# Kernel tuning notes

Hardware: AMD Instinct MI355X
Metric: run time of the kernel (lower is better)

## Reference

```python
import jax, jax.numpy as jnp
import numpy as np

B, N, NT, C, CO = 8, 12288, 3072, 256, 512
H0, W0 = 128, 96

def _grid_idx(loc, h, w):
    # loc in [-1,1] -> nearest grid cell index (matches token2map's round/clamp)
    loc = jnp.clip(jax.lax.stop_gradient(loc), -1.0, 1.0)
    xi = jnp.clip(jnp.round(0.5 * (loc[..., 0] + 1.0) * w - 0.5).astype(jnp.int32), 0, w - 1)
    yi = jnp.clip(jnp.round(0.5 * (loc[..., 1] + 1.0) * h - 0.5).astype(jnp.int32), 0, h - 1)
    return xi + yi * w

def _bn(x, gamma, beta):
    # BatchNorm (training-mode batch stats) over (B, N) per channel; x: (B, N, C)
    mean = x.mean(axis=(0, 1))
    var = ((x - mean) ** 2).mean(axis=(0, 1))
    return (x - mean) * jax.lax.rsqrt(var + 1e-5) * gamma + beta

def _token2map(x, loc, idx_agg, h, w):
    b, n, c = x.shape
    n0 = idx_agg.shape[1]
    seg = (_grid_idx(loc, h, w) + jnp.arange(b)[:, None] * (h * w)).reshape(-1)
    x_pt = jnp.take_along_axis(x, idx_agg[..., None], axis=1).reshape(b * n0, c)
    summed = jax.ops.segment_sum(x_pt, seg, num_segments=b * h * w)
    count = jax.ops.segment_sum(jnp.ones((b * n0,), x.dtype), seg, num_segments=b * h * w)
    x_map = summed / (count + 1e-6)[:, None]
    return x_map.reshape(b, h, w, c).transpose(0, 3, 1, 2)  # (B, C, H, W)

def _map2token(fmap, nt, loc, idx_agg_t, agg_weight_t):
    b, c, h, w = fmap.shape
    n0 = idx_agg_t.shape[1]
    idx_hw = _grid_idx(loc, h, w)
    fflat = fmap.reshape(b, c, h * w).transpose(0, 2, 1)  # (B, HW, C)
    feat = jnp.take_along_axis(fflat, idx_hw[..., None], axis=1)  # (B, N0, C)
    wgt = agg_weight_t.reshape(b, n0)
    seg = (idx_agg_t + jnp.arange(b)[:, None] * nt).reshape(-1)
    num = jax.ops.segment_sum((feat * wgt[..., None]).reshape(b * n0, c), seg, num_segments=b * nt)
    den = jax.ops.segment_sum(wgt.reshape(-1), seg, num_segments=b * nt) + 1e-6
    return (num / den[:, None]).reshape(b, nt, c)

def _token_downup(x_s, idx_agg_s, nt, idx_agg_t, agg_weight_t):
    b, s, c = x_s.shape
    n0 = idx_agg_s.shape[1]
    x_pt = jnp.take_along_axis(x_s, idx_agg_s[..., None], axis=1)  # (B, N0, C)
    wgt = agg_weight_t.reshape(b, n0)
    seg = (idx_agg_t + jnp.arange(b)[:, None] * nt).reshape(-1)
    num = jax.ops.segment_sum((x_pt * wgt[..., None]).reshape(b * n0, c), seg, num_segments=b * nt)
    den = jax.ops.segment_sum(wgt.reshape(-1), seg, num_segments=b * nt) + 1e-6
    return (num / den[:, None]).reshape(b, nt, c)

def setup_inputs():
    key = jax.random.key(0)
    ks = jax.random.split(key, 10)
    return {
        "x": jax.random.normal(ks[0], (B, N, C), jnp.float32),
        "loc_orig": jax.random.uniform(ks[1], (B, N, 2), jnp.float32, -1.0, 1.0),
        "idx_agg": jax.random.randint(ks[2], (B, N), 0, N),
        "agg_weight": jax.random.uniform(ks[3], (B, N, 1), jnp.float32),
        "x_t": jax.random.normal(ks[4], (B, NT, C), jnp.float32),
        "idx_agg_t": jax.random.randint(ks[5], (B, N), 0, NT),
        "agg_weight_t": jax.random.uniform(ks[6], (B, N, 1), jnp.float32),
        "H": H0, "W": W0,
        "dw_conv_w": jax.random.normal(ks[7], (C, 1, 3, 3), jnp.float32) * 0.1,
        "dw_skip_w": jax.random.normal(ks[8], (C, 1, 1, 1), jnp.float32) * 0.1,
        "norm1_gamma": jnp.ones((C,), jnp.float32),
        "norm1_beta": jnp.zeros((C,), jnp.float32),
        "conv_w": jax.random.normal(ks[9], (CO, C), jnp.float32) * (1.0 / np.sqrt(C)),
        "norm2_gamma": jnp.ones((CO,), jnp.float32),
        "norm2_beta": jnp.zeros((CO,), jnp.float32),
    }

def reference(x, loc_orig, idx_agg, agg_weight, x_t, idx_agg_t, agg_weight_t, H, W,
              dw_conv_w, dw_skip_w, norm1_gamma, norm1_beta, conv_w, norm2_gamma, norm2_beta):
    nt = x_t.shape[1]
    # token2map -> depthwise 3x3 stride-2 conv -> map2token (onto downsampled grid)
    x_map = _token2map(x, loc_orig, idx_agg, H, W)
    x_map = jax.lax.conv_general_dilated(
        x_map, dw_conv_w, window_strides=(2, 2), padding=((1, 1), (1, 1)),
        feature_group_count=x_map.shape[1],
        dimension_numbers=("NCHW", "OIHW", "NCHW"))
    x_map = _map2token(x_map, nt, loc_orig, idx_agg_t, agg_weight_t)
    # skip path: token_downup + 1x1 depthwise (per-channel scale)
    xd = _token_downup(x, idx_agg, nt, idx_agg_t, agg_weight_t)
    xd = xd * dw_skip_w.reshape(1, 1, -1)
    xd = xd + x_map
    xd = _bn(xd, norm1_gamma, norm1_beta)
    xd = jnp.einsum("bnc,oc->bno", xd, conv_w)  # 1x1 conv C -> CO
    xd = _bn(xd, norm2_gamma, norm2_beta)
    return jax.nn.relu(xd)
```

## Files before the change

### kernel.cpp

```cpp
#include <hip/hip_runtime.h>
#include <hip/hip_bf16.h>

using bf16 = __hip_bfloat16;
typedef __attribute__((ext_vector_type(8))) short bf16x8;
typedef __attribute__((ext_vector_type(4))) float f32x4;

#define BB   8
#define NN   12288
#define NTOK (BB*NN)
#define NTK  3072
#define CC   256
#define CCO  512
#define HH   128
#define WWI  96
#define HWIN (HH*WWI)
#define H2   64
#define W2   48
#define HW2  (H2*W2)
#define RR   (BB*NTK)

#define O_CONV  0LL
#define O_XD    6291456LL
#define O_AUX   9437184LL
#define O_WT    12582912LL
#define O_ST1   12713984LL
#define O_ST2   12714496LL
#define O_AB1   12715520LL
#define O_B2    12716032LL
#define O_AB2   12716544LL
#define O_FLAG  12717568LL
#define O_META  12717572LL
#define O_OFF   12914180LL
#define O_LIST  13037060LL

__device__ __forceinline__ float cvt(float v){ return v; }
__device__ __forceinline__ float cvt(bf16 v){ return __bfloat162float(v); }
template<typename T>
__device__ __forceinline__ float ld(const void* p, long long i){
    return cvt(((const T*)p)[i]);
}
__device__ __forceinline__ float bfu(unsigned short u){
    return __uint_as_float((unsigned)u << 16);
}
__device__ __forceinline__ unsigned short ubf(float f){
    bf16 h = __float2bfloat16(f);
    return *(unsigned short*)&h;
}
template<typename T>
__device__ __forceinline__ f32x4 ld4(const void* p, long long i);
template<>
__device__ __forceinline__ f32x4 ld4<bf16>(const void* p, long long i){
    const ushort4 u = *(const ushort4*)((const unsigned short*)p + i);
    return (f32x4){bfu(u.x), bfu(u.y), bfu(u.z), bfu(u.w)};
}
template<>
__device__ __forceinline__ f32x4 ld4<float>(const void* p, long long i){
    const float4 v = *(const float4*)((const float*)p + i);
    return (f32x4){v.x, v.y, v.z, v.w};
}

__global__ void k_flag(const float* __restrict__ locf, float* __restrict__ flag){
    if (threadIdx.x == 0){
        int bad = 0;
        for (int i = 0; i < 64; ++i){
            const float v = locf[i];
            if (!(v >= -1.0f && v <= 1.0f)) bad = 1;
        }
        flag[0] = bad ? 1.0f : 0.0f;
    }
}

__device__ __forceinline__ int2 gidx2(float lx, float ly, int h, int w){
    lx = fminf(fmaxf(lx, -1.f), 1.f);
    ly = fminf(fmaxf(ly, -1.f), 1.f);
    int xi = (int)rintf(0.5f*(lx+1.f)*(float)w - 0.5f);
    int yi = (int)rintf(0.5f*(ly+1.f)*(float)h - 0.5f);
    xi = min(max(xi,0), w-1); yi = min(max(yi,0), h-1);
    return make_int2(xi, yi);
}

template<typename T>
__device__ void meta_body(const void* loc, const int* __restrict__ iat, const void* wt,
                          int2* __restrict__ meta, int* __restrict__ off){
    const int tok = blockIdx.x*256 + threadIdx.x;
    const int b = tok / NN;
    const float lx = ld<T>(loc, 2LL*tok);
    const float ly = ld<T>(loc, 2LL*tok + 1);
    const int2 g1 = gidx2(lx, ly, HH, WWI);
    const int2 g2 = gidx2(lx, ly, H2, W2);
    const float wv = ld<T>(wt, tok);
    int2 m; m.x = g2.x + g2.y*W2; m.y = __float_as_int(wv);
    meta[tok] = m;
    atomicAdd(&off[b*HWIN + g1.x + g1.y*WWI], 1);
    atomicAdd(&off[NTOK + b*NTK + iat[tok]], 1);
}
__global__ __launch_bounds__(256) void k_meta(
        const void* loc, const int* __restrict__ iat, const void* wt,
        const float* __restrict__ flag, int2* __restrict__ meta,
        int* __restrict__ off){
    if (flag[0] != 0.0f) meta_body<bf16>(loc, iat, wt, meta, off);
    else                 meta_body<float>(loc, iat, wt, meta, off);
}

#define SCN  (NTOK + RR)
#define SCB  120
__global__ __launch_bounds__(1024) void k_scan1(int* __restrict__ off, int* __restrict__ aux){
    __shared__ int sm[1024];
    const int tid = threadIdx.x;
    const int gid = blockIdx.x*1024 + tid;
    const int v = off[gid];
    sm[tid] = v;
    __syncthreads();
    for (int d = 1; d < 1024; d <<= 1){
        const int t = (tid >= d) ? sm[tid-d] : 0;
        __syncthreads();
        sm[tid] += t;
        __syncthreads();
    }
    off[gid] = sm[tid] - v;
    if (tid == 1023) aux[blockIdx.x] = sm[1023];
}
__global__ __launch_bounds__(128) void k_scan2(int* __restrict__ aux){
    __shared__ int sm[128];
    const int tid = threadIdx.x;
    const int v = (tid < SCB) ? aux[tid] : 0;
    sm[tid] = v;
    __syncthreads();
    for (int d = 1; d < 128; d <<= 1){
        const int t = (tid >= d) ? sm[tid-d] : 0;
        __syncthreads();
        sm[tid] += t;
        __syncthreads();
    }
    if (tid < SCB) aux[tid] = sm[tid] - v;
}
__global__ __launch_bounds__(1024) void k_scan3(int* __restrict__ off, const int* __restrict__ aux){
    off[blockIdx.x*1024 + threadIdx.x] += aux[blockIdx.x];
}

template<typename T>
__device__ void fill_body(const void* loc, const int* __restrict__ ia,
                          const int* __restrict__ iat,
                          int* __restrict__ off, int* __restrict__ list){
    const int tok = blockIdx.x*256 + threadIdx.x;
    const int b = tok / NN;
    const float lx = ld<T>(loc, 2LL*tok);
    const float ly = ld<T>(loc, 2LL*tok + 1);
    const int2 g1 = gidx2(lx, ly, HH, WWI);
    const int pa = atomicAdd(&off[b*HWIN + g1.x + g1.y*WWI], 1);
    list[pa] = b*NN + ia[tok];
    const int pb = atomicAdd(&off[NTOK + b*NTK + iat[tok]], 1);
    list[pb] = tok;
}
__global__ __launch_bounds__(256) void k_fill(
        const void* loc, const int* __restrict__ ia, const int* __restrict__ iat,
        const float* __restrict__ flag,
        int* __restrict__ off, int* __restrict__ list){
    if (flag[0] != 0.0f) fill_body<bf16>(loc, ia, iat, off, list);
    else                 fill_body<float>(loc, ia, iat, off, list);
}

template<typename T>
__device__ void conv_body(const void* x, const void* dww,
                          const int* __restrict__ off, const int* __restrict__ list,
                          bf16* __restrict__ conv){
    __shared__ f32x4 red[3][64];
    const int tid = threadIdx.x;
    const int kh = tid >> 6;
    const int lane = tid & 63;
    const int ch0 = lane*4;
    const int cell = blockIdx.x;
    const int b = cell / HW2;
    const int p = cell % HW2;
    const int oh = p / W2, ow = p % W2;
    const int ih = 2*oh - 1 + kh;
    f32x4 part = (f32x4){0.f,0.f,0.f,0.f};
    if (ih >= 0){
        const int gbase = b*HWIN + ih*WWI + 2*ow - 1;
        const int e0 = (gbase >= 0) ? off[gbase] : 0;
        const int e1 = off[gbase+1];
        const int e2 = off[gbase+2];
        const int ms = (ow > 0) ? off[gbase-1] : e0;
        f32x4 w0, w1, w2;
        #pragma unroll
        for (int c = 0; c < 4; ++c){
            w0[c] = ld<T>(dww, (long long)(ch0+c)*9 + kh*3 + 0);
            w1[c] = ld<T>(dww, (long long)(ch0+c)*9 + kh*3 + 1);
            w2[c] = ld<T>(dww, (long long)(ch0+c)*9 + kh*3 + 2);
        }
        f32x4 b0 = (f32x4){0.f,0.f,0.f,0.f};
        f32x4 b1 = (f32x4){0.f,0.f,0.f,0.f};
        f32x4 b2 = (f32x4){0.f,0.f,0.f,0.f};
        int idx = ms;
        while (idx < e2){
            const int cnt = min(e2 - idx, 64);
            const int tokv = (lane < cnt) ? list[idx + lane] : 0;
            int j = 0;
            for (; j + 4 <= cnt; j += 4){
                int oxs[4];
                #pragma unroll
                for (int u = 0; u < 4; ++u)
                    oxs[u] = __shfl(tokv, j+u)*CC + ch0;
                f32x4 xv[4];
                #pragma unroll
                for (int u = 0; u < 4; ++u) xv[u] = ld4<T>(x, (long long)oxs[u]);
                #pragma unroll
                for (int u = 0; u < 4; ++u){
                    const int gi = idx + j + u;
                    if (gi < e0)      b0 += xv[u];
                    else if (gi < e1) b1 += xv[u];
                    else              b2 += xv[u];
                }
            }
            for (; j < cnt; ++j){
                const f32x4 xv = ld4<T>(x, (long long)(__shfl(tokv, j)*CC + ch0));
                const int gi = idx + j;
                if (gi < e0)      b0 += xv;
                else if (gi < e1) b1 += xv;
                else              b2 += xv;
            }
            idx += cnt;
        }
        const float r0 = 1.0f/((float)(e0 - ms) + 1e-6f);
        const float r1 = 1.0f/((float)(e1 - e0) + 1e-6f);
        const float r2 = 1.0f/((float)(e2 - e1) + 1e-6f);
        #pragma unroll
        for (int c = 0; c < 4; ++c)
            part[c] = w0[c]*b0[c]*r0 + w1[c]*b1[c]*r1 + w2[c]*b2[c]*r2;
    }
    red[kh][lane] = part;
    __syncthreads();
    if (kh == 0){
        const f32x4 t0 = red[0][lane];
        const f32x4 t1 = red[1][lane];
        const f32x4 t2 = red[2][lane];
        ushort4 o;
        o.x = ubf(t0[0]+t1[0]+t2[0]);
        o.y = ubf(t0[1]+t1[1]+t2[1]);
        o.z = ubf(t0[2]+t1[2]+t2[2]);
        o.w = ubf(t0[3]+t1[3]+t2[3]);
        *(ushort4*)((unsigned short*)conv + (long long)cell*CC + ch0) = o;
    }
}
__global__ __launch_bounds__(192) void k_conv(
        const void* x, const void* dww, const float* __restrict__ flag,
        const int* __restrict__ off, const int* __restrict__ list,
        bf16* __restrict__ conv){
    if (flag[0] != 0.0f) conv_body<bf16>(x, dww, off, list, conv);
    else                 conv_body<float>(x, dww, off, list, conv);
}

#define TGW 2
template<typename T>
__device__ void num_body(const void* x, const bf16* __restrict__ conv,
                         const void* skw, const int* __restrict__ ia,
                         const int2* __restrict__ meta,
                         const int* __restrict__ off, const int* __restrict__ list,
                         bf16* __restrict__ xdf, float* __restrict__ st1){
    __shared__ float ss[CC], sq[CC];
    const int tid = threadIdx.x;
    ss[tid] = 0.f; sq[tid] = 0.f;
    __syncthreads();
    const int wave = tid >> 6;
    const int lane = tid & 63;
    const int ch0 = lane*4;
    const f32x4 sk = ld4<T>(skw, ch0);
    const int W = blockIdx.x*4 + wave;
    const int gt0 = W*TGW;
    const int b = gt0 / NTK;
    int offv = 0;
    if (lane <= TGW) offv = off[NTOK + gt0 - 1 + lane];
    const int s0  = __shfl(offv, 0);
    const int eb0 = __shfl(offv, 1);
    const int eb1 = __shfl(offv, 2);
    f32x4 a0 = (f32x4){0.f,0.f,0.f,0.f};
    f32x4 a1 = (f32x4){0.f,0.f,0.f,0.f};
    float d0 = 0.f, d1 = 0.f;
    int idx = s0;
    while (idx < eb1){
        const int cnt = min(eb1 - idx, 64);
        int tok = 0, ja = 0; int2 m = make_int2(0, 0);
        if (lane < cnt){
            tok = list[idx + lane];
            m = meta[tok];
            ja = ia[tok];
        }
        int j = 0;
        for (; j + 4 <= cnt; j += 4){
            float wv[4]; int ox[4], oc[4];
            #pragma unroll
            for (int u = 0; u < 4; ++u){
                wv[u] = __int_as_float(__shfl(m.y, j+u));
                ox[u] = (b*NN  + __shfl(ja,  j+u))*CC + ch0;
                oc[u] = (b*HW2 + __shfl(m.x, j+u))*CC + ch0;
            }
            f32x4 xv[4], cv[4];
            #pragma unroll
            for (int u = 0; u < 4; ++u) xv[u] = ld4<T>(x, (long long)ox[u]);
            #pragma unroll
            for (int u = 0; u < 4; ++u) cv[u] = ld4<bf16>(conv, (long long)oc[u]);
            #pragma unroll
            for (int u = 0; u < 4; ++u){
                f32x4 cb;
                #pragma unroll
                for (int c = 0; c < 4; ++c) cb[c] = wv[u]*(sk[c]*xv[u][c] + cv[u][c]);
                if (idx + j + u < eb0){ a0 += cb; d0 += wv[u]; }
                else                  { a1 += cb; d1 += wv[u]; }
            }
        }
        for (; j < cnt; ++j){
            const float wv = __int_as_float(__shfl(m.y, j));
            const int ox = (b*NN  + __shfl(ja,  j))*CC + ch0;
            const int oc = (b*HW2 + __shfl(m.x, j))*CC + ch0;
            const f32x4 xv = ld4<T>(x, (long long)ox);
            const f32x4 cv = ld4<bf16>(conv, (long long)oc);
            f32x4 cb;
            #pragma unroll
            for (int c = 0; c < 4; ++c) cb[c] = wv*(sk[c]*xv[c] + cv[c]);
            if (idx + j < eb0){ a0 += cb; d0 += wv; }
            else              { a1 += cb; d1 += wv; }
        }
        idx += cnt;
    }
    float sa0=0.f,sa1=0.f,sa2=0.f,sa3=0.f, qa0=0.f,qa1=0.f,qa2=0.f,qa3=0.f;
    #pragma unroll
    for (int t = 0; t < TGW; ++t){
        const f32x4 a  = (t == 0) ? a0 : a1;
        const float dn = (t == 0) ? d0 : d1;
        const int gt = gt0 + t;
        const float rl = 1.0f/(dn + 1e-6f);
        const float v0 = a[0]*rl, v1 = a[1]*rl, v2 = a[2]*rl, v3 = a[3]*rl;
        ushort4 o; o.x = ubf(v0); o.y = ubf(v1); o.z = ubf(v2); o.w = ubf(v3);
        const long long bi = (long long)(gt >> 4)*4096 + (long long)(ch0 >> 3)*128
                           + (long long)(gt & 15)*8 + (ch0 & 7);
        *(ushort4*)((unsigned short*)xdf + bi) = o;
        sa0 += v0; sa1 += v1; sa2 += v2; sa3 += v3;
        qa0 += v0*v0; qa1 += v1*v1; qa2 += v2*v2; qa3 += v3*v3;
    }
    atomicAdd(&ss[ch0  ], sa0); atomicAdd(&sq[ch0  ], qa0);
    atomicAdd(&ss[ch0+1], sa1); atomicAdd(&sq[ch0+1], qa1);
    atomicAdd(&ss[ch0+2], sa2); atomicAdd(&sq[ch0+2], qa2);
    atomicAdd(&ss[ch0+3], sa3); atomicAdd(&sq[ch0+3], qa3);
    __syncthreads();
    atomicAdd(&st1[tid], ss[tid]);
    atomicAdd(&st1[CC + tid], sq[tid]);
}
__global__ __launch_bounds__(256) void k_num(
        const void* x, const bf16* __restrict__ conv, const void* skw,
        const int* __restrict__ ia, const int2* __restrict__ meta,
        const int* __restrict__ off, const int* __restrict__ list,
        const float* __restrict__ flag,
        bf16* __restrict__ xdf, float* __restrict__ st1){
    if (flag[0] != 0.0f) num_body<bf16>(x, conv, skw, ia, meta, off, list, xdf, st1);
    else                 num_body<float>(x, conv, skw, ia, meta, off, list, xdf, st1);
}

template<typename T>
__device__ void bn1_body(const float* __restrict__ st1, const void* g1, const void* b1,
                         float* __restrict__ ab1){
    const int tid = threadIdx.x;
    const float mean = st1[tid]/(float)RR;
    const float var  = st1[CC + tid]/(float)RR - mean*mean;
    const float a  = ld<T>(g1, tid) * rsqrtf(var + 1e-5f);
    ab1[tid] = a;
    ab1[CC + tid] = ld<T>(b1, tid) - mean*a;
}
__global__ __launch_bounds__(256) void k_bn1(
        const float* __restrict__ st1, const void* g1, const void* b1,
        const float* __restrict__ flag, float* __restrict__ ab1){
    if (flag[0] != 0.0f) bn1_body<bf16>(st1, g1, b1, ab1);
    else                 bn1_body<float>(st1, g1, b1, ab1);
}

template<typename T>
__device__ void wt_body(const void* cw, const float* __restrict__ ab1,
                        bf16* __restrict__ wTf, float* __restrict__ bias2){
    const int c = blockIdx.x, o = threadIdx.x;
    const float w = ld<T>(cw, (long long)o*CC + c);
    wTf[(((long long)(o >> 4)*32 + (c >> 3))*16 + (o & 15))*8 + (c & 7)] =
        __float2bfloat16(w * ab1[c]);
    atomicAdd(&bias2[o], w * ab1[CC + c]);
}
__global__ __launch_bounds__(512) void k_wt(
        const void* cw, const float* __restrict__ ab1,
        const float* __restrict__ flag, bf16* __restrict__ wTf,
        float* __restrict__ bias2){
    if (flag[0] != 0.0f) wt_body<bf16>(cw, ab1, wTf, bias2);
    else                 wt_body<float>(cw, ab1, wTf, bias2);
}

__global__ __launch_bounds__(256) void k_gemm(
        const bf16* __restrict__ xdf, const bf16* __restrict__ wTf,
        const float* __restrict__ bias2, const float* __restrict__ flag,
        void* __restrict__ y, float* __restrict__ st2){
    __shared__ float ss[128], sq[128];
    const int tid = threadIdx.x;
    if (tid < 128){ ss[tid] = 0.f; sq[tid] = 0.f; }
    __syncthreads();
    const int wave = tid >> 6;
    const int lane = tid & 63;
    const int l16 = lane & 15;
    const int lq  = lane >> 4;
    const int mb = blockIdx.x;
    const int nb = blockIdx.y;
    const int mt = mb*4 + wave;
    const int n0t = nb*8;
    const short* ap = (const short*)xdf + ((long long)mt*32 + lq)*128 + (long long)l16*8;
    const short* bp = (const short*)wTf + ((long long)n0t*32 + lq)*128 + (long long)l16*8;
    f32x4 acc[8];
    #pragma unroll
    for (int nt = 0; nt < 8; ++nt) acc[nt] = (f32x4){0.f,0.f,0.f,0.f};
    #pragma unroll
    for (int kg0 = 0; kg0 < 8; ++kg0){
        const bf16x8 af = *((const bf16x8*)(ap + kg0*512));
        #pragma unroll
        for (int nt = 0; nt < 8; ++nt){
            const bf16x8 bfr = *((const bf16x8*)(bp + (long long)nt*4096 + kg0*512));
            acc[nt] = __builtin_amdgcn_mfma_f32_16x16x32_bf16(af, bfr, acc[nt], 0, 0, 0);
        }
    }
    const int row0 = mt*16 + lq*4;
    const bool isbf = (flag[0] != 0.0f);
    #pragma unroll
    for (int nt = 0; nt < 8; ++nt){
        const int col = nb*128 + nt*16 + l16;
        const float bz = bias2[col];
        float s = 0.f, q = 0.f;
        float v[4];
        #pragma unroll
        for (int r = 0; r < 4; ++r){
            v[r] = acc[nt][r] + bz;
            s += v[r]; q += v[r]*v[r];
        }
        if (isbf){
            bf16* yo = (bf16*)y;
            #pragma unroll
            for (int r = 0; r < 4; ++r)
                yo[(long long)(row0 + r)*CCO + col] = __float2bfloat16(v[r]);
        } else {
            float* yo = (float*)y;
            #pragma unroll
            for (int r = 0; r < 4; ++r)
                yo[(long long)(row0 + r)*CCO + col] = v[r];
        }
        s += __shfl_xor(s, 16); s += __shfl_xor(s, 32);
        q += __shfl_xor(q, 16); q += __shfl_xor(q, 32);
        if (lq == 0){
            atomicAdd(&ss[nt*16 + l16], s);
            atomicAdd(&sq[nt*16 + l16], q);
        }
    }
    __syncthreads();
    if (tid < 128){
        atomicAdd(&st2[nb*128 + tid], ss[tid]);
        atomicAdd(&st2[CCO + nb*128 + tid], sq[tid]);
    }
}

template<typename T>
__device__ void bn2_body(const float* __restrict__ st2, const void* g2, const void* b2,
                         float* __restrict__ ab2){
    const int tid = threadIdx.x;
    const float mean = st2[tid]/(float)RR;
    const float var  = st2[CCO + tid]/(float)RR - mean*mean;
    const float a = ld<T>(g2, tid) * rsqrtf(var + 1e-5f);
    ab2[tid] = a;
    ab2[CCO + tid] = ld<T>(b2, tid) - mean*a;
}
__global__ __launch_bounds__(512) void k_bn2(
        const float* __restrict__ st2, const void* g2, const void* b2,
        const float* __restrict__ flag, float* __restrict__ ab2){
    if (flag[0] != 0.0f) bn2_body<bf16>(st2, g2, b2, ab2);
    else                 bn2_body<float>(st2, g2, b2, ab2);
}

__global__ __launch_bounds__(256) void k_out(
        void* __restrict__ y, const float* __restrict__ ab2,
        const float* __restrict__ flag){
    const long long i0 = ((long long)blockIdx.x*256 + threadIdx.x)*4;
    const int o0 = (int)(i0 & (CCO-1));
    if (flag[0] != 0.0f){
        unsigned short* p = (unsigned short*)y;
        ushort4 u = *(ushort4*)(p + i0);
        float v0 = bfu(u.x)*ab2[o0  ] + ab2[CCO + o0  ];
        float v1 = bfu(u.y)*ab2[o0+1] + ab2[CCO + o0+1];
        float v2 = bfu(u.z)*ab2[o0+2] + ab2[CCO + o0+2];
        float v3 = bfu(u.w)*ab2[o0+3] + ab2[CCO + o0+3];
        u.x = ubf(fmaxf(v0,0.f)); u.y = ubf(fmaxf(v1,0.f));
        u.z = ubf(fmaxf(v2,0.f)); u.w = ubf(fmaxf(v3,0.f));
        *(ushort4*)(p + i0) = u;
    } else {
        float* p = (float*)y;
        float4 v = *(float4*)(p + i0);
        v.x = fmaxf(v.x*ab2[o0  ] + ab2[CCO + o0  ], 0.f);
        v.y = fmaxf(v.y*ab2[o0+1] + ab2[CCO + o0+1], 0.f);
        v.z = fmaxf(v.z*ab2[o0+2] + ab2[CCO + o0+2], 0.f);
        v.w = fmaxf(v.w*ab2[o0+3] + ab2[CCO + o0+3], 0.f);
        *(float4*)(p + i0) = v;
    }
}

extern "C" void kernel_launch(void* const* d_in, const int* in_sizes, int n_in,
                              void* d_out, int out_size, void* d_ws, size_t ws_size,
                              hipStream_t stream){
    (void)in_sizes; (void)n_in; (void)out_size; (void)ws_size;
    const void* x   = d_in[0];
    const void* loc = d_in[1];
    const int*  ia  = (const int*)d_in[2];
    const int*  iat = (const int*)d_in[5];
    const void* wt  = d_in[6];
    const void* dww = d_in[9];
    const void* skw = d_in[10];
    const void* g1  = d_in[11];
    const void* b1  = d_in[12];
    const void* cw  = d_in[13];
    const void* g2  = d_in[14];
    const void* b2  = d_in[15];
    float* ws = (float*)d_ws;
    float* flag = ws + O_FLAG;
    int*  off  = (int*)(ws + O_OFF);
    int*  list = (int*)(ws + O_LIST);
    int*  aux  = (int*)(ws + O_AUX);
    int2* meta = (int2*)(ws + O_META);
    bf16* conv = (bf16*)(ws + O_CONV);
    bf16* xdf  = (bf16*)(ws + O_XD);
    bf16* wTf  = (bf16*)(ws + O_WT);

    hipMemsetAsync(ws + O_ST1, 0, (size_t)2560*4, stream);
    hipMemsetAsync(off, 0, (size_t)SCN*4, stream);

    k_flag<<<dim3(1), dim3(64), 0, stream>>>((const float*)loc, flag);

    k_meta<<<dim3(NTOK/256), dim3(256), 0, stream>>>(loc, iat, wt, flag, meta, off);

    k_scan1<<<dim3(SCB), dim3(1024), 0, stream>>>(off, aux);
    k_scan2<<<dim3(1), dim3(128), 0, stream>>>(aux);
    k_scan3<<<dim3(SCB), dim3(1024), 0, stream>>>(off, aux);

    k_fill<<<dim3(NTOK/256), dim3(256), 0, stream>>>(loc, ia, iat, flag, off, list);

    k_conv<<<dim3(BB*HW2), dim3(192), 0, stream>>>(x, dww, flag, off, list, conv);

    k_num<<<dim3(RR/(4*TGW)), dim3(256), 0, stream>>>(
        x, conv, skw, ia, meta, off, list, flag, xdf, ws + O_ST1);

    k_bn1<<<dim3(1), dim3(256), 0, stream>>>(
        ws + O_ST1, g1, b1, flag, ws + O_AB1);

    k_wt<<<dim3(CC), dim3(512), 0, stream>>>(cw, ws + O_AB1, flag, wTf, ws + O_B2);

    k_gemm<<<dim3(384, 4), dim3(256), 0, stream>>>(
        xdf, wTf, ws + O_B2, flag, d_out, ws + O_ST2);

    k_bn2<<<dim3(1), dim3(512), 0, stream>>>(ws + O_ST2, g2, b2, flag, ws + O_AB2);

    k_out<<<dim3((RR*CCO)/1024, 1), dim3(256), 0, stream>>>(d_out, ws + O_AB2, flag);
}
```

Measured before the change: 405.0 us.

## Split BN1 stats into separate kernel and spread BN2 atomics across slots

k_num drops its per-block shared-memory and global atomic accumulation of BN1 statistics, processes four target tokens per wave sequentially with a simpler unrolled-free inner loop, and a new k_st1 kernel re-reads xdf to compute channel sums. The GEMM's BN2 statistic atomics are spread over 8 partial slots indexed by row block to reduce global atomic contention, and k_bn2 sums the slots. The trade is an extra launch and an extra pass over xdf, plus loss of the 4-way load unrolling in the gather loop, in exchange for less atomic contention.

Measured after the change: 358.1 us. 11.6% less time.

```diff
diff --git a/kernel.cpp b/kernel.cpp
--- a/kernel.cpp
+++ b/kernel.cpp
@@ -22,6 +22,7 @@
 #define O_CONV  0LL
 #define O_XD    6291456LL
 #define O_AUX   9437184LL
+#define O_ST2P  9437440LL
 #define O_WT    12582912LL
 #define O_ST1   12713984LL
 #define O_ST2   12714496LL
@@ -250,109 +251,99 @@
     else                 conv_body<float>(x, dww, off, list, conv);
 }
 
-#define TGW 2
+#define TGW 4
 template<typename T>
 __device__ void num_body(const void* x, const bf16* __restrict__ conv,
                          const void* skw, const int* __restrict__ ia,
                          const int2* __restrict__ meta,
                          const int* __restrict__ off, const int* __restrict__ list,
-                         bf16* __restrict__ xdf, float* __restrict__ st1){
-    __shared__ float ss[CC], sq[CC];
-    const int tid = threadIdx.x;
-    ss[tid] = 0.f; sq[tid] = 0.f;
-    __syncthreads();
+                         bf16* __restrict__ xdf){
+    const int tid = threadIdx.x;
     const int wave = tid >> 6;
     const int lane = tid & 63;
     const int ch0 = lane*4;
     const f32x4 sk = ld4<T>(skw, ch0);
     const int W = blockIdx.x*4 + wave;
-    const int gt0 = W*TGW;
-    const int b = gt0 / NTK;
-    int offv = 0;
-    if (lane <= TGW) offv = off[NTOK + gt0 - 1 + lane];
-    const int s0  = __shfl(offv, 0);
-    const int eb0 = __shfl(offv, 1);
-    const int eb1 = __shfl(offv, 2);
-    f32x4 a0 = (f32x4){0.f,0.f,0.f,0.f};
-    f32x4 a1 = (f32x4){0.f,0.f,0.f,0.f};
-    float d0 = 0.f, d1 = 0.f;
-    int idx = s0;
-    while (idx < eb1){
-        const int cnt = min(eb1 - idx, 64);
-        int tok = 0, ja = 0; int2 m = make_int2(0, 0);
-        if (lane < cnt){
-            tok = list[idx + lane];
-            m = meta[tok];
-            ja = ia[tok];
-        }
-        int j = 0;
-        for (; j + 4 <= cnt; j += 4){
-            float wv[4]; int ox[4], oc[4];
-            #pragma unroll
-            for (int u = 0; u < 4; ++u){
-                wv[u] = __int_as_float(__shfl(m.y, j+u));
-                ox[u] = (b*NN  + __shfl(ja,  j+u))*CC + ch0;
-                oc[u] = (b*HW2 + __shfl(m.x, j+u))*CC + ch0;
+    for (int t = 0; t < TGW; ++t){
+        const int gt = W*TGW + t;
+        const int b = gt / NTK;
+        const int gj = NTOK + gt;
+        const int e  = off[gj];
+        const int s  = off[gj-1];
+        f32x4 a = (f32x4){0.f,0.f,0.f,0.f};
+        float den = 0.f;
+        int idx = s;
+        while (idx < e){
+            const int cnt = min(e - idx, 64);
+            int tok = 0, ja = 0; int2 m = make_int2(0, 0);
+            if (lane < cnt){
+                tok = list[idx + lane];
+                m = meta[tok];
+                ja = ia[tok];
             }
-            f32x4 xv[4], cv[4];
-            #pragma unroll
-            for (int u = 0; u < 4; ++u) xv[u] = ld4<T>(x, (long long)ox[u]);
-            #pragma unroll
-            for (int u = 0; u < 4; ++u) cv[u] = ld4<bf16>(conv, (long long)oc[u]);
-            #pragma unroll
-            for (int u = 0; u < 4; ++u){
-                f32x4 cb;
+            for (int j = 0; j < cnt; ++j){
+                const float wv = __int_as_float(__shfl(m.y, j));
+                const int rx = b*NN  + __shfl(ja, j);
+                const int rc = b*HW2 + __shfl(m.x, j);
+                const f32x4 xv = ld4<T>(x, (long long)rx*CC + ch0);
+                const f32x4 cv = ld4<bf16>(conv, (long long)rc*CC + ch0);
                 #pragma unroll
-                for (int c = 0; c < 4; ++c) cb[c] = wv[u]*(sk[c]*xv[u][c] + cv[u][c]);
-                if (idx + j + u < eb0){ a0 += cb; d0 += wv[u]; }
-                else                  { a1 += cb; d1 += wv[u]; }
+                for (int c = 0; c < 4; ++c)
+                    a[c] += wv*(sk[c]*xv[c] + cv[c]);
+                den += wv;
             }
-        }
-        for (; j < cnt; ++j){
-            const float wv = __int_as_float(__shfl(m.y, j));
-            const int ox = (b*NN  + __shfl(ja,  j))*CC + ch0;
-            const int oc = (b*HW2 + __shfl(m.x, j))*CC + ch0;
-            const f32x4 xv = ld4<T>(x, (long long)ox);
-            const f32x4 cv = ld4<bf16>(conv, (long long)oc);
-            f32x4 cb;
-            #pragma unroll
-            for (int c = 0; c < 4; ++c) cb[c] = wv*(sk[c]*xv[c] + cv[c]);
-            if (idx + j < eb0){ a0 += cb; d0 += wv; }
-            else              { a1 += cb; d1 += wv; }
-        }
-        idx += cnt;
-    }
-    float sa0=0.f,sa1=0.f,sa2=0.f,sa3=0.f, qa0=0.f,qa1=0.f,qa2=0.f,qa3=0.f;
-    #pragma unroll
-    for (int t = 0; t < TGW; ++t){
-        const f32x4 a  = (t == 0) ? a0 : a1;
-        const float dn = (t == 0) ? d0 : d1;
-        const int gt = gt0 + t;
-        const float rl = 1.0f/(dn + 1e-6f);
-        const float v0 = a[0]*rl, v1 = a[1]*rl, v2 = a[2]*rl, v3 = a[3]*rl;
-        ushort4 o; o.x = ubf(v0); o.y = ubf(v1); o.z = ubf(v2); o.w = ubf(v3);
+            idx += cnt;
+        }
+        const float rl = 1.0f/(den + 1e-6f);
+        ushort4 o;
+        o.x = ubf(a[0]*rl); o.y = ubf(a[1]*rl);
+        o.z = ubf(a[2]*rl); o.w = ubf(a[3]*rl);
         const long long bi = (long long)(gt >> 4)*4096 + (long long)(ch0 >> 3)*128
                            + (long long)(gt & 15)*8 + (ch0 & 7);
         *(ushort4*)((unsigned short*)xdf + bi) = o;
-        sa0 += v0; sa1 += v1; sa2 += v2; sa3 += v3;
-        qa0 += v0*v0; qa1 += v1*v1; qa2 += v2*v2; qa3 += v3*v3;
-    }
-    atomicAdd(&ss[ch0  ], sa0); atomicAdd(&sq[ch0  ], qa0);
-    atomicAdd(&ss[ch0+1], sa1); atomicAdd(&sq[ch0+1], qa1);
-    atomicAdd(&ss[ch0+2], sa2); atomicAdd(&sq[ch0+2], qa2);
-    atomicAdd(&ss[ch0+3], sa3); atomicAdd(&sq[ch0+3], qa3);
-    __syncthreads();
-    atomicAdd(&st1[tid], ss[tid]);
-    atomicAdd(&st1[CC + tid], sq[tid]);
+    }
 }
 __global__ __launch_bounds__(256) void k_num(
         const void* x, const bf16* __restrict__ conv, const void* skw,
         const int* __restrict__ ia, const int2* __restrict__ meta,
         const int* __restrict__ off, const int* __restrict__ list,
         const float* __restrict__ flag,
-        bf16* __restrict__ xdf, float* __restrict__ st1){
-    if (flag[0] != 0.0f) num_body<bf16>(x, conv, skw, ia, meta, off, list, xdf, st1);
-    else                 num_body<float>(x, conv, skw, ia, meta, off, list, xdf, st1);
+        bf16* __restrict__ xdf){
+    if (flag[0] != 0.0f) num_body<bf16>(x, conv, skw, ia, meta, off, list, xdf);
+    else                 num_body<float>(x, conv, skw, ia, meta, off, list, xdf);
+}
+
+__global__ __launch_bounds__(512) void k_st1(const bf16* __restrict__ xdf,
+                                             float* __restrict__ st1){
+    __shared__ float ss[CC], sq[CC];
+    const int tid = threadIdx.x;
+    if (tid < CC){ ss[tid] = 0.f; sq[tid] = 0.f; }
+    __syncthreads();
+    const int tl = tid & 15;
+    const int cg = tid >> 4;
+    const int c0 = cg*8;
+    float s[8], q[8];
+    #pragma unroll
+    for (int k = 0; k < 8; ++k){ s[k] = 0.f; q[k] = 0.f; }
+    for (int sb = blockIdx.x; sb < RR/16; sb += gridDim.x){
+        const long long o = (long long)sb*512 + cg*16 + tl;
+        const bf16x8 v = *((const bf16x8*)xdf + o);
+        #pragma unroll
+        for (int k = 0; k < 8; ++k){
+            const float f = bfu((unsigned short)v[k]);
+            s[k] += f; q[k] += f*f;
+        }
+    }
+    #pragma unroll
+    for (int k = 0; k < 8; ++k){
+        atomicAdd(&ss[c0+k], s[k]);
+        atomicAdd(&sq[c0+k], q[k]);
+    }
+    __syncthreads();
+    if (tid < CC){
+        atomicAdd(&st1[tid], ss[tid]);
+        atomicAdd(&st1[CC + tid], sq[tid]);
+    }
 }
 
 template<typename T>
@@ -392,7 +383,7 @@
 __global__ __launch_bounds__(256) void k_gemm(
         const bf16* __restrict__ xdf, const bf16* __restrict__ wTf,
         const float* __restrict__ bias2, const float* __restrict__ flag,
-        void* __restrict__ y, float* __restrict__ st2){
+        void* __restrict__ y, float* __restrict__ st2p){
     __shared__ float ss[128], sq[128];
     const int tid = threadIdx.x;
     if (tid < 128){ ss[tid] = 0.f; sq[tid] = 0.f; }
@@ -452,26 +443,33 @@
     }
     __syncthreads();
     if (tid < 128){
-        atomicAdd(&st2[nb*128 + tid], ss[tid]);
-        atomicAdd(&st2[CCO + nb*128 + tid], sq[tid]);
-    }
-}
-
-template<typename T>
-__device__ void bn2_body(const float* __restrict__ st2, const void* g2, const void* b2,
+        const int slot = (mb & 7)*1024;
+        atomicAdd(&st2p[slot + nb*128 + tid], ss[tid]);
+        atomicAdd(&st2p[slot + 512 + nb*128 + tid], sq[tid]);
+    }
+}
+
+template<typename T>
+__device__ void bn2_body(const float* __restrict__ st2p, const void* g2, const void* b2,
                          float* __restrict__ ab2){
     const int tid = threadIdx.x;
-    const float mean = st2[tid]/(float)RR;
-    const float var  = st2[CCO + tid]/(float)RR - mean*mean;
+    float s = 0.f, q = 0.f;
+    #pragma unroll
+    for (int p = 0; p < 8; ++p){
+        s += st2p[p*1024 + tid];
+        q += st2p[p*1024 + 512 + tid];
+    }
+    const float mean = s/(float)RR;
+    const float var  = q/(float)RR - mean*mean;
     const float a = ld<T>(g2, tid) * rsqrtf(var + 1e-5f);
     ab2[tid] = a;
     ab2[CCO + tid] = ld<T>(b2, tid) - mean*a;
 }
 __global__ __launch_bounds__(512) void k_bn2(
-        const float* __restrict__ st2, const void* g2, const void* b2,
+        const float* __restrict__ st2p, const void* g2, const void* b2,
         const float* __restrict__ flag, float* __restrict__ ab2){
-    if (flag[0] != 0.0f) bn2_body<bf16>(st2, g2, b2, ab2);
-    else                 bn2_body<float>(st2, g2, b2, ab2);
+    if (flag[0] != 0.0f) bn2_body<bf16>(st2p, g2, b2, ab2);
+    else                 bn2_body<float>(st2p, g2, b2, ab2);
 }
 
 __global__ __launch_bounds__(256) void k_out(
@@ -527,6 +525,7 @@
     bf16* wTf  = (bf16*)(ws + O_WT);
 
     hipMemsetAsync(ws + O_ST1, 0, (size_t)2560*4, stream);
+    hipMemsetAsync(ws + O_ST2P, 0, (size_t)8192*4, stream);
     hipMemsetAsync(off, 0, (size_t)SCN*4, stream);
 
     k_flag<<<dim3(1), dim3(64), 0, stream>>>((const float*)loc, flag);
@@ -542,7 +541,9 @@
     k_conv<<<dim3(BB*HW2), dim3(192), 0, stream>>>(x, dww, flag, off, list, conv);
 
     k_num<<<dim3(RR/(4*TGW)), dim3(256), 0, stream>>>(
-        x, conv, skw, ia, meta, off, list, flag, xdf, ws + O_ST1);
+        x, conv, skw, ia, meta, off, list, flag, xdf);
+
+    k_st1<<<dim3(192), dim3(512), 0, stream>>>(xdf, ws + O_ST1);
 
     k_bn1<<<dim3(1), dim3(256), 0, stream>>>(
         ws + O_ST1, g1, b1, flag, ws + O_AB1);
@@ -550,9 +551,9 @@
     k_wt<<<dim3(CC), dim3(512), 0, stream>>>(cw, ws + O_AB1, flag, wTf, ws + O_B2);
 
     k_gemm<<<dim3(384, 4), dim3(256), 0, stream>>>(
-        xdf, wTf, ws + O_B2, flag, d_out, ws + O_ST2);
-
-    k_bn2<<<dim3(1), dim3(512), 0, stream>>>(ws + O_ST2, g2, b2, flag, ws + O_AB2);
+        xdf, wTf, ws + O_B2, flag, d_out, ws + O_ST2P);
+
+    k_bn2<<<dim3(1), dim3(512), 0, stream>>>(ws + O_ST2P, g2, b2, flag, ws + O_AB2);
 
     k_out<<<dim3((RR*CCO)/1024, 1), dim3(256), 0, stream>>>(d_out, ws + O_AB2, flag);
 }
```
